# Performance work log

Hardware: AMD Instinct MI355X
Metric: run time of the kernel (lower is better)

## Reference

```python
import jax, jax.numpy as jnp
import numpy as np

D_MODEL = 256; N_HEADS = 8; N_LEVELS = 4; N_POINTS = 4; D_FF = 2048
SHAPES = [(128, 128), (64, 64), (32, 32), (16, 16)]  # (H_l, W_l) per level
LV = sum(h * w for h, w in SHAPES)  # 21760
B = 8; NQ = 900
EPS = 1e-5


def layer_norm(x, s, b):
    m = x.mean(-1, keepdims=True)
    v = x.var(-1, keepdims=True)
    return (x - m) * jax.lax.rsqrt(v + EPS) * s + b


def mha(q, k, v, in_w, in_b, out_w, out_b):
    # torch nn.MultiheadAttention, batch_first, eval mode (no dropout)
    Bq, Lq, C = q.shape
    h = N_HEADS; d = C // h
    wq, wk, wv = jnp.split(in_w, 3, axis=0)
    bq, bk, bv = jnp.split(in_b, 3)
    qh = (q @ wq.T + bq).reshape(Bq, Lq, h, d)
    kh = (k @ wk.T + bk).reshape(Bq, -1, h, d)
    vh = (v @ wv.T + bv).reshape(Bq, -1, h, d)
    scale = jnp.asarray(1.0 / np.sqrt(d), q.dtype)
    attn = jax.nn.softmax(jnp.einsum('bqhd,bkhd->bhqk', qh, kh) * scale, axis=-1)
    o = jnp.einsum('bhqk,bkhd->bqhd', attn, vh).reshape(Bq, Lq, C)
    return o @ out_w.T + out_b


def deform_attn(query, ref, memory, spatial_shapes, val_w, val_b, off_w, off_b, aw_w, aw_b, co_w, co_b):
    # MSDeformAttn forward (eval): offsets/weights from query, bilinear sample value per level/point
    Bq, Lq, C = query.shape
    h, L, P = N_HEADS, N_LEVELS, N_POINTS
    dh = C // h
    value = (memory @ val_w.T + val_b).reshape(Bq, -1, h, dh)  # (B, Lv, h, dh)
    off = (query @ off_w.T + off_b).reshape(Bq, Lq, h, L, P, 2)
    aw = jax.nn.softmax((query @ aw_w.T + aw_b).reshape(Bq, Lq, h, L * P), axis=-1)
    aw = aw.reshape(Bq, Lq, h, L, P)
    # normalizer = (W_l, H_l) per level
    normalizer = spatial_shapes[:, ::-1].astype(query.dtype)
    loc = ref[:, :, None, :, None, :] + off / normalizer[None, None, None, :, None, :]  # (B,Lq,h,L,P,2)
    out = jnp.zeros((Bq, h, Lq, dh), query.dtype)
    start = 0
    for l, (Hl, Wl) in enumerate(SHAPES):
        v_l = value[:, start:start + Hl * Wl].transpose(0, 2, 1, 3)  # (B,h,Hl*Wl,dh)
        start += Hl * Wl
        xy = loc[:, :, :, l]  # (B,Lq,h,P,2) normalized in [0,1]
        # grid_sample align_corners=False pixel coords
        x = xy[..., 0] * Wl - 0.5
        y = xy[..., 1] * Hl - 0.5
        x0 = jnp.floor(x); y0 = jnp.floor(y)
        wx = x - x0; wy = y - y0
        acc = jnp.zeros((Bq, h, Lq * P, dh), query.dtype)
        for dx, dy, w in ((0, 0, (1 - wx) * (1 - wy)), (1, 0, wx * (1 - wy)),
                          (0, 1, (1 - wx) * wy), (1, 1, wx * wy)):
            xi = x0 + dx; yi = y0 + dy
            valid = (xi >= 0) & (xi <= Wl - 1) & (yi >= 0) & (yi <= Hl - 1)
            xi = jnp.clip(xi, 0, Wl - 1).astype(jnp.int32)
            yi = jnp.clip(yi, 0, Hl - 1).astype(jnp.int32)
            idx = (yi * Wl + xi).transpose(0, 2, 1, 3).reshape(Bq, h, Lq * P)
            g = jnp.take_along_axis(v_l, idx[..., None], axis=2)  # (B,h,Lq*P,dh)
            wgt = (w * valid).transpose(0, 2, 1, 3).reshape(Bq, h, Lq * P)
            acc = acc + g * wgt[..., None]
        acc = acc.reshape(Bq, h, Lq, P, dh)
        wl = aw[:, :, :, l].transpose(0, 2, 1, 3)  # (B,h,Lq,P)
        out = out + jnp.einsum('bhqpd,bhqp->bhqd', acc, wl)
    out = out.transpose(0, 2, 1, 3).reshape(Bq, Lq, C)
    return out @ co_w.T + co_b


def forward(tgt, memory, query_pos, reference_points, sa_in_w, sa_in_b, sa_out_w, sa_out_b,
            off_w, off_b, aw_w, aw_b, val_w, val_b, co_w, co_b,
            l1_w, l1_b, l2_w, l2_b, ln1_s, ln1_b, ln2_s, ln2_b, ln3_s, ln3_b, spatial_shapes):
    q = tgt + query_pos  # with_pos_embed; eval mode: no group_detr split, no dropout
    tgt2 = mha(q, q, tgt, sa_in_w, sa_in_b, sa_out_w, sa_out_b)
    tgt = layer_norm(tgt + tgt2, ln1_s, ln1_b)
    tgt2 = deform_attn(tgt + query_pos, reference_points, memory, spatial_shapes,
                       val_w, val_b, off_w, off_b, aw_w, aw_b, co_w, co_b)
    tgt = layer_norm(tgt + tgt2, ln2_s, ln2_b)
    tgt2 = jax.nn.relu(tgt @ l1_w.T + l1_b) @ l2_w.T + l2_b
    return layer_norm(tgt + tgt2, ln3_s, ln3_b)


def setup_inputs():
    key = jax.random.key(0)
    ks = jax.random.split(key, 16)
    C = D_MODEL
    f = lambda i, shape, s=0.02: jax.random.normal(ks[i], shape, jnp.float32) * s
    HLP = N_HEADS * N_LEVELS * N_POINTS
    return {
        'tgt': f(0, (B, NQ, C), 1.0),
        'memory': f(1, (B, LV, C), 1.0),
        'query_pos': f(2, (B, NQ, C), 1.0),
        'reference_points': jax.random.uniform(ks[3], (B, NQ, N_LEVELS, 2), jnp.float32),
        'sa_in_w': f(4, (3 * C, C)), 'sa_in_b': jnp.zeros((3 * C,), jnp.float32),
        'sa_out_w': f(5, (C, C)), 'sa_out_b': jnp.zeros((C,), jnp.float32),
        'off_w': f(6, (HLP * 2, C)), 'off_b': f(7, (HLP * 2,), 0.5),
        'aw_w': f(8, (HLP, C)), 'aw_b': jnp.zeros((HLP,), jnp.float32),
        'val_w': f(9, (C, C)), 'val_b': jnp.zeros((C,), jnp.float32),
        'co_w': f(10, (C, C)), 'co_b': jnp.zeros((C,), jnp.float32),
        'l1_w': f(11, (D_FF, C)), 'l1_b': jnp.zeros((D_FF,), jnp.float32),
        'l2_w': f(12, (C, D_FF)), 'l2_b': jnp.zeros((C,), jnp.float32),
        'ln1_s': jnp.ones((C,), jnp.float32), 'ln1_b': jnp.zeros((C,), jnp.float32),
        'ln2_s': jnp.ones((C,), jnp.float32), 'ln2_b': jnp.zeros((C,), jnp.float32),
        'ln3_s': jnp.ones((C,), jnp.float32), 'ln3_b': jnp.zeros((C,), jnp.float32),
        'spatial_shapes': jnp.asarray(SHAPES, jnp.int32),
        'level_start_index': jnp.asarray(np.cumsum([0] + [h * w for h, w in SHAPES[:-1]]), jnp.int32),
    }


def reference(tgt, memory, query_pos, reference_points, sa_in_w, sa_in_b, sa_out_w, sa_out_b,
              off_w, off_b, aw_w, aw_b, val_w, val_b, co_w, co_b,
              l1_w, l1_b, l2_w, l2_b, ln1_s, ln1_b, ln2_s, ln2_b, ln3_s, ln3_b,
              spatial_shapes, level_start_index):
    return forward(tgt, memory, query_pos, reference_points, sa_in_w, sa_in_b, sa_out_w, sa_out_b,
                   off_w, off_b, aw_w, aw_b, val_w, val_b, co_w, co_b,
                   l1_w, l1_b, l2_w, l2_b, ln1_s, ln1_b, ln2_s, ln2_b, ln3_s, ln3_b, spatial_shapes)
```

## Files before the change

### kernel.cpp

```cpp
#include <hip/hip_runtime.h>
#include <hip/hip_bf16.h>

#define NQL 900
#define CDIM 256
#define BDIM 8
#define LVTOT 21760

typedef __bf16 bf16x8 __attribute__((ext_vector_type(8)));
typedef float f32x4 __attribute__((ext_vector_type(4)));
typedef uint u32x4 __attribute__((ext_vector_type(4)));
typedef uint u32x2 __attribute__((ext_vector_type(2)));

__device__ __forceinline__ ushort f2bf(float x) {
  uint u = __builtin_bit_cast(uint, x);
  u += 0x7fff + ((u >> 16) & 1);
  return (ushort)(u >> 16);
}

template <bool ABF16, bool AADD, bool RELU, bool OUTBF16>
__global__ __launch_bounds__(256, 4) void mgemm_kernel(const void* __restrict__ Ap,
                                                       const float* __restrict__ A2p,
                                                       const float* __restrict__ W,
                                                       const float* __restrict__ bias,
                                                       void* __restrict__ Cout,
                                                       int M, int N, int K) {
  __shared__ ushort smem[10240];
  ushort* As = smem;
  ushort* Bs = smem + 5120;
  const int tid = threadIdx.x;
  const int m0 = blockIdx.y * 128, n0 = blockIdx.x * 128;
  const int wv = tid >> 6;
  const int wm = (wv >> 1) * 64, wn = (wv & 1) * 64;
  const int lane = tid & 63;
  const int lr = lane & 15, kq = lane >> 4;

  f32x4 acc[4][4] = {};
  float4 pa[2][2], pb[2][2];
  u32x4 pa16[2];

  auto load_tiles = [&](int k0) {
#pragma unroll
    for (int it = 0; it < 2; ++it) {
      int idx = it * 256 + tid;
      int r = idx >> 2, s = (idx & 3) << 3;
      int gm = min(m0 + r, M - 1);
      if constexpr (ABF16) {
        pa16[it] = *(const u32x4*)((const ushort*)Ap + (size_t)gm * K + k0 + s);
      } else {
        const float* ap = (const float*)Ap + (size_t)gm * K + k0 + s;
        pa[it][0] = *(const float4*)ap;
        pa[it][1] = *(const float4*)(ap + 4);
        if constexpr (AADD) {
          const float* ap2 = A2p + (size_t)gm * K + k0 + s;
          float4 q0 = *(const float4*)ap2;
          float4 q1 = *(const float4*)(ap2 + 4);
          pa[it][0].x += q0.x; pa[it][0].y += q0.y; pa[it][0].z += q0.z; pa[it][0].w += q0.w;
          pa[it][1].x += q1.x; pa[it][1].y += q1.y; pa[it][1].z += q1.z; pa[it][1].w += q1.w;
        }
      }
      int gn = min(n0 + r, N - 1);
      const float* wp = W + (size_t)gn * K + k0 + s;
      pb[it][0] = *(const float4*)wp;
      pb[it][1] = *(const float4*)(wp + 4);
    }
  };

  auto store_tiles = [&]() {
#pragma unroll
    for (int it = 0; it < 2; ++it) {
      int idx = it * 256 + tid;
      int r = idx >> 2, s = (idx & 3) << 3;
      u32x4 u;
      if constexpr (ABF16) {
        u = pa16[it];
      } else {
        u.x = f2bf(pa[it][0].x) | ((uint)f2bf(pa[it][0].y) << 16);
        u.y = f2bf(pa[it][0].z) | ((uint)f2bf(pa[it][0].w) << 16);
        u.z = f2bf(pa[it][1].x) | ((uint)f2bf(pa[it][1].y) << 16);
        u.w = f2bf(pa[it][1].z) | ((uint)f2bf(pa[it][1].w) << 16);
      }
      *(u32x4*)&As[r * 40 + s] = u;
      u32x4 w;
      w.x = f2bf(pb[it][0].x) | ((uint)f2bf(pb[it][0].y) << 16);
      w.y = f2bf(pb[it][0].z) | ((uint)f2bf(pb[it][0].w) << 16);
      w.z = f2bf(pb[it][1].x) | ((uint)f2bf(pb[it][1].y) << 16);
      w.w = f2bf(pb[it][1].z) | ((uint)f2bf(pb[it][1].w) << 16);
      *(u32x4*)&Bs[r * 40 + s] = w;
    }
  };

  load_tiles(0);
  for (int k0 = 0; k0 < K; k0 += 32) {
    store_tiles();
    __syncthreads();
    if (k0 + 32 < K) load_tiles(k0 + 32);
    bf16x8 af[4], bq[4];
#pragma unroll
    for (int m = 0; m < 4; ++m)
      af[m] = __builtin_bit_cast(bf16x8, *(const u32x4*)&As[(wm + m * 16 + lr) * 40 + kq * 8]);
#pragma unroll
    for (int n = 0; n < 4; ++n)
      bq[n] = __builtin_bit_cast(bf16x8, *(const u32x4*)&Bs[(wn + n * 16 + lr) * 40 + kq * 8]);
#pragma unroll
    for (int m = 0; m < 4; ++m)
#pragma unroll
      for (int n = 0; n < 4; ++n)
        acc[m][n] = __builtin_amdgcn_mfma_f32_16x16x32_bf16(af[m], bq[n], acc[m][n], 0, 0, 0);
    __syncthreads();
  }

  if constexpr (OUTBF16) {
    ushort* Cs = smem;
#pragma unroll
    for (int p = 0; p < 2; ++p) {
      __syncthreads();
      if (wm == p * 64) {
#pragma unroll
        for (int n = 0; n < 4; ++n) {
          int col = wn + n * 16 + lr;
          float bv = bias[n0 + col];
#pragma unroll
          for (int m = 0; m < 4; ++m)
#pragma unroll
            for (int j = 0; j < 4; ++j) {
              float v = acc[m][n][j] + bv;
              if (RELU) v = fmaxf(v, 0.f);
              Cs[(m * 16 + kq * 4 + j) * 136 + col] = f2bf(v);
            }
        }
      }
      __syncthreads();
#pragma unroll
      for (int it = 0; it < 4; ++it) {
        int idx = it * 256 + tid;
        int r = idx >> 4, c = (idx & 15) * 8;
        int grow = m0 + p * 64 + r;
        if (grow < M) {
          u32x4 u = *(const u32x4*)&Cs[r * 136 + c];
          *(u32x4*)((ushort*)Cout + (size_t)grow * N + n0 + c) = u;
        }
      }
    }
  } else {
#pragma unroll
    for (int n = 0; n < 4; ++n) {
      int gcol = n0 + wn + n * 16 + lr;
      float bv = bias[gcol];
#pragma unroll
      for (int m = 0; m < 4; ++m) {
        int rbase = m0 + wm + m * 16 + kq * 4;
#pragma unroll
        for (int j = 0; j < 4; ++j) {
          int grow = rbase + j;
          if (grow >= M) continue;
          float v = acc[m][n][j] + bv;
          if (RELU) v = fmaxf(v, 0.f);
          ((float*)Cout)[(size_t)grow * N + gcol] = v;
        }
      }
    }
  }
}

template <bool ABF16, bool AADD, bool RELU, bool HASRES, bool OUTBF16>
__global__ __launch_bounds__(256, 4) void mgemm64_kernel(const void* __restrict__ Ap,
                                                         const float* __restrict__ A2p,
                                                         const float* __restrict__ W,
                                                         const float* __restrict__ bias,
                                                         const float* __restrict__ Rres,
                                                         void* __restrict__ Cout,
                                                         int M, int N, int K) {
  __shared__ ushort smem[5120];
  ushort* As = smem;
  ushort* Bs = smem + 2560;
  const int tid = threadIdx.x;
  const int m0 = blockIdx.y * 64, n0 = blockIdx.x * 64;
  const int wv = tid >> 6, lane = tid & 63;
  const int wm = (wv >> 1) * 32, wn = (wv & 1) * 32;
  const int lr = lane & 15, kq = lane >> 4;

  f32x4 acc[2][2] = {};
  float4 pa[2], pb[2];
  u32x4 pa16;

  auto load_tiles = [&](int k0) {
    int r = tid >> 2, s = (tid & 3) << 3;
    int gm = min(m0 + r, M - 1);
    if constexpr (ABF16) {
      pa16 = *(const u32x4*)((const ushort*)Ap + (size_t)gm * K + k0 + s);
    } else {
      const float* ap = (const float*)Ap + (size_t)gm * K + k0 + s;
      pa[0] = *(const float4*)ap;
      pa[1] = *(const float4*)(ap + 4);
      if constexpr (AADD) {
        const float* ap2 = A2p + (size_t)gm * K + k0 + s;
        float4 q0 = *(const float4*)ap2;
        float4 q1 = *(const float4*)(ap2 + 4);
        pa[0].x += q0.x; pa[0].y += q0.y; pa[0].z += q0.z; pa[0].w += q0.w;
        pa[1].x += q1.x; pa[1].y += q1.y; pa[1].z += q1.z; pa[1].w += q1.w;
      }
    }
    int gn = min(n0 + r, N - 1);
    const float* wp = W + (size_t)gn * K + k0 + s;
    pb[0] = *(const float4*)wp;
    pb[1] = *(const float4*)(wp + 4);
  };

  auto store_tiles = [&]() {
    int r = tid >> 2, s = (tid & 3) << 3;
    u32x4 u;
    if constexpr (ABF16) {
      u = pa16;
    } else {
      u.x = f2bf(pa[0].x) | ((uint)f2bf(pa[0].y) << 16);
      u.y = f2bf(pa[0].z) | ((uint)f2bf(pa[0].w) << 16);
      u.z = f2bf(pa[1].x) | ((uint)f2bf(pa[1].y) << 16);
      u.w = f2bf(pa[1].z) | ((uint)f2bf(pa[1].w) << 16);
    }
    *(u32x4*)&As[r * 40 + s] = u;
    u32x4 w;
    w.x = f2bf(pb[0].x) | ((uint)f2bf(pb[0].y) << 16);
    w.y = f2bf(pb[0].z) | ((uint)f2bf(pb[0].w) << 16);
    w.z = f2bf(pb[1].x) | ((uint)f2bf(pb[1].y) << 16);
    w.w = f2bf(pb[1].z) | ((uint)f2bf(pb[1].w) << 16);
    *(u32x4*)&Bs[r * 40 + s] = w;
  };

  load_tiles(0);
  for (int k0 = 0; k0 < K; k0 += 32) {
    store_tiles();
    __syncthreads();
    if (k0 + 32 < K) load_tiles(k0 + 32);
    bf16x8 af[2], bq[2];
#pragma unroll
    for (int m = 0; m < 2; ++m)
      af[m] = __builtin_bit_cast(bf16x8, *(const u32x4*)&As[(wm + m * 16 + lr) * 40 + kq * 8]);
#pragma unroll
    for (int n = 0; n < 2; ++n)
      bq[n] = __builtin_bit_cast(bf16x8, *(const u32x4*)&Bs[(wn + n * 16 + lr) * 40 + kq * 8]);
#pragma unroll
    for (int m = 0; m < 2; ++m)
#pragma unroll
      for (int n = 0; n < 2; ++n)
        acc[m][n] = __builtin_amdgcn_mfma_f32_16x16x32_bf16(af[m], bq[n], acc[m][n], 0, 0, 0);
    __syncthreads();
  }

  if constexpr (OUTBF16) {
    ushort* Cs = smem;
    __syncthreads();
#pragma unroll
    for (int n = 0; n < 2; ++n) {
      int col = wn + n * 16 + lr;
      float bv = bias[n0 + col];
#pragma unroll
      for (int m = 0; m < 2; ++m)
#pragma unroll
        for (int j = 0; j < 4; ++j) {
          float v = acc[m][n][j] + bv;
          if (RELU) v = fmaxf(v, 0.f);
          Cs[(wm + m * 16 + kq * 4 + j) * 72 + col] = f2bf(v);
        }
    }
    __syncthreads();
#pragma unroll
    for (int it = 0; it < 2; ++it) {
      int idx = it * 256 + tid;
      int r = idx >> 3, c = (idx & 7) * 8;
      int grow = m0 + r;
      if (grow < M) {
        u32x4 u = *(const u32x4*)&Cs[r * 72 + c];
        *(u32x4*)((ushort*)Cout + (size_t)grow * N + n0 + c) = u;
      }
    }
  } else {
#pragma unroll
    for (int n = 0; n < 2; ++n) {
      int gcol = n0 + wn + n * 16 + lr;
      float bv = bias[gcol];
#pragma unroll
      for (int m = 0; m < 2; ++m) {
        int rbase = m0 + wm + m * 16 + kq * 4;
#pragma unroll
        for (int j = 0; j < 4; ++j) {
          int grow = rbase + j;
          if (grow >= M) continue;
          float v = acc[m][n][j] + bv;
          if (HASRES) v += Rres[(size_t)grow * N + gcol];
          if (RELU) v = fmaxf(v, 0.f);
          ((float*)Cout)[(size_t)grow * N + gcol] = v;
        }
      }
    }
  }
}

template <bool ABF16, bool OUTBF16>
__global__ __launch_bounds__(256, 2) void mgemm256_kernel(const void* __restrict__ Ap,
                                                          const float* __restrict__ W,
                                                          const float* __restrict__ bias,
                                                          void* __restrict__ Cout,
                                                          int M, int K) {
  __shared__ ushort smem[16896];
  ushort* As = smem;
  ushort* Bs = smem + 2560;
  const int tid = threadIdx.x;
  const int m0 = blockIdx.x * 64;
  const int wv = tid >> 6;
  const int lane = tid & 63;
  const int lr = lane & 15, kq = lane >> 4;

  f32x4 acc[16] = {};
  float4 pa[2];
  u32x4 pa16;
  float4 pb[4][2];

  auto load_tiles = [&](int k0) {
    {
      int r = tid >> 2, s = (tid & 3) << 3;
      int gm = min(m0 + r, M - 1);
      if constexpr (ABF16) {
        pa16 = *(const u32x4*)((const ushort*)Ap + (size_t)gm * K + k0 + s);
      } else {
        const float* ap = (const float*)Ap + (size_t)gm * K + k0 + s;
        pa[0] = *(const float4*)ap;
        pa[1] = *(const float4*)(ap + 4);
      }
    }
#pragma unroll
    for (int it = 0; it < 4; ++it) {
      int idx = it * 256 + tid;
      int r = idx >> 2, s = (idx & 3) << 3;
      const float* wp = W + (size_t)r * K + k0 + s;
      pb[it][0] = *(const float4*)wp;
      pb[it][1] = *(const float4*)(wp + 4);
    }
  };

  auto store_tiles = [&]() {
    {
      int r = tid >> 2, s = (tid & 3) << 3;
      u32x4 u;
      if constexpr (ABF16) {
        u = pa16;
      } else {
        u.x = f2bf(pa[0].x) | ((uint)f2bf(pa[0].y) << 16);
        u.y = f2bf(pa[0].z) | ((uint)f2bf(pa[0].w) << 16);
        u.z = f2bf(pa[1].x) | ((uint)f2bf(pa[1].y) << 16);
        u.w = f2bf(pa[1].z) | ((uint)f2bf(pa[1].w) << 16);
      }
      *(u32x4*)&As[r * 40 + s] = u;
    }
#pragma unroll
    for (int it = 0; it < 4; ++it) {
      int idx = it * 256 + tid;
      int r = idx >> 2, s = (idx & 3) << 3;
      u32x4 w;
      w.x = f2bf(pb[it][0].x) | ((uint)f2bf(pb[it][0].y) << 16);
      w.y = f2bf(pb[it][0].z) | ((uint)f2bf(pb[it][0].w) << 16);
      w.z = f2bf(pb[it][1].x) | ((uint)f2bf(pb[it][1].y) << 16);
      w.w = f2bf(pb[it][1].z) | ((uint)f2bf(pb[it][1].w) << 16);
      *(u32x4*)&Bs[r * 40 + s] = w;
    }
  };

  load_tiles(0);
  for (int k0 = 0; k0 < K; k0 += 32) {
    store_tiles();
    __syncthreads();
    if (k0 + 32 < K) load_tiles(k0 + 32);
    bf16x8 af = __builtin_bit_cast(bf16x8, *(const u32x4*)&As[(wv * 16 + lr) * 40 + kq * 8]);
#pragma unroll
    for (int ng = 0; ng < 16; ++ng) {
      bf16x8 bq = __builtin_bit_cast(bf16x8, *(const u32x4*)&Bs[(ng * 16 + lr) * 40 + kq * 8]);
      acc[ng] = __builtin_amdgcn_mfma_f32_16x16x32_bf16(af, bq, acc[ng], 0, 0, 0);
    }
    __syncthreads();
  }

  if constexpr (OUTBF16) {
    ushort* Cs = smem;
#pragma unroll
    for (int nf = 0; nf < 16; ++nf) {
      int col = nf * 16 + lr;
      float bv = bias[col];
#pragma unroll
      for (int j = 0; j < 4; ++j) {
        int row = wv * 16 + kq * 4 + j;
        Cs[row * 264 + col] = f2bf(acc[nf][j] + bv);
      }
    }
    __syncthreads();
#pragma unroll
    for (int it = 0; it < 8; ++it) {
      int idx = it * 256 + tid;
      int r = idx >> 5, c = (idx & 31) * 8;
      int grow = m0 + r;
      if (grow < M) {
        u32x4 u = *(const u32x4*)&Cs[r * 264 + c];
        *(u32x4*)((ushort*)Cout + (size_t)grow * 256 + c) = u;
      }
    }
  } else {
#pragma unroll
    for (int nf = 0; nf < 16; ++nf) {
      int col = nf * 16 + lr;
      float bv = bias[col];
#pragma unroll
      for (int j = 0; j < 4; ++j) {
        int grow = m0 + wv * 16 + kq * 4 + j;
        if (grow < M)
          ((float*)Cout)[(size_t)grow * 256 + col] = acc[nf][j] + bv;
      }
    }
  }
}

__global__ __launch_bounds__(256) void vt_kernel(const ushort* __restrict__ tmp_v,
                                                 ushort* __restrict__ vt) {
  __shared__ ushort Ls[64 * 40];
  const int qt = blockIdx.x;
  const int bh = blockIdx.y;
  const int b = bh >> 3, h = bh & 7;
  const int tid = threadIdx.x;
  const int q0 = qt * 64;
  {
    int r = tid >> 2, c = (tid & 3) * 8;
    int gq = min(q0 + r, NQL - 1);
    u32x4 u = *(const u32x4*)(tmp_v + ((size_t)(b * NQL + gq) * 256) + h * 32 + c);
    *(u32x4*)&Ls[r * 40 + c] = u;
  }
  __syncthreads();
  {
    int d = tid >> 3, qw = (tid & 7) * 8;
    u32x4 u;
    uint w[8];
#pragma unroll
    for (int j = 0; j < 8; ++j) w[j] = Ls[(qw + j) * 40 + d];
    u.x = w[0] | (w[1] << 16);
    u.y = w[2] | (w[3] << 16);
    u.z = w[4] | (w[5] << 16);
    u.w = w[6] | (w[7] << 16);
    *(u32x4*)(vt + ((size_t)(bh * 32 + d) * 960) + q0 + qw) = u;
  }
}

__global__ __launch_bounds__(256, 2) void fattn_kernel(const ushort* __restrict__ qk,
                                                       const ushort* __restrict__ vt,
                                                       float* __restrict__ out) {
  __shared__ ushort Ks[64 * 40];
  __shared__ ushort Vs[32 * 72];
  __shared__ ushort Ps[4][16 * 72];
  const int qt = blockIdx.x, bh = blockIdx.y;
  const int b = bh >> 3, h = bh & 7;
  const int tid = threadIdx.x;
  const int wv = tid >> 6, lane = tid & 63;
  const int lq = lane & 15, hi = lane >> 4;
  const int q0 = qt * 64 + wv * 16;
  const float SC = 0.17677669529663689f;

  bf16x8 qfrag;
  {
    int qrow = min(q0 + lq, NQL - 1);
    qfrag = __builtin_bit_cast(bf16x8,
        *(const u32x4*)(qk + (size_t)(b * NQL + qrow) * 512 + h * 32 + hi * 8));
  }

  f32x4 o0 = {}, o1 = {};
  float mrow = -1e30f, lrow = 0.f;

  for (int kt = 0; kt < 15; ++kt) {
    const int k0 = kt * 64;
    __syncthreads();
    {
      int r = tid >> 2, c = (tid & 3) * 8;
      int gk = min(k0 + r, NQL - 1);
      u32x4 u = *(const u32x4*)(qk + (size_t)(b * NQL + gk) * 512 + 256 + h * 32 + c);
      *(u32x4*)&Ks[r * 40 + c] = u;
    }
    {
      int r = tid >> 3, c = (tid & 7) * 8;
      u32x4 u = *(const u32x4*)(vt + (size_t)(bh * 32 + r) * 960 + k0 + c);
      *(u32x4*)&Vs[r * 72 + c] = u;
    }
    __syncthreads();

    f32x4 st[4];
#pragma unroll
    for (int mt = 0; mt < 4; ++mt) {
      bf16x8 kf = __builtin_bit_cast(bf16x8, *(const u32x4*)&Ks[(mt * 16 + lq) * 40 + hi * 8]);
      f32x4 z = {};
      st[mt] = __builtin_amdgcn_mfma_f32_16x16x32_bf16(kf, qfrag, z, 0, 0, 0);
    }
    float sv[4][4];
    float lmax = -1e30f;
#pragma unroll
    for (int mt = 0; mt < 4; ++mt)
#pragma unroll
      for (int j = 0; j < 4; ++j) {
        int key = k0 + mt * 16 + hi * 4 + j;
        float v = st[mt][j] * SC;
        v = (key < NQL) ? v : -1e30f;
        sv[mt][j] = v;
        lmax = fmaxf(lmax, v);
      }
    lmax = fmaxf(lmax, __shfl_xor(lmax, 16));
    lmax = fmaxf(lmax, __shfl_xor(lmax, 32));
    float mnew = fmaxf(mrow, lmax);
    float rs = __expf(mrow - mnew);
    float lsum = 0.f;
    uint pw[4][2];
#pragma unroll
    for (int mt = 0; mt < 4; ++mt) {
      float p0 = __expf(sv[mt][0] - mnew);
      float p1 = __expf(sv[mt][1] - mnew);
      float p2 = __expf(sv[mt][2] - mnew);
      float p3 = __expf(sv[mt][3] - mnew);
      lsum += (p0 + p1) + (p2 + p3);
      pw[mt][0] = f2bf(p0) | ((uint)f2bf(p1) << 16);
      pw[mt][1] = f2bf(p2) | ((uint)f2bf(p3) << 16);
    }
    lsum += __shfl_xor(lsum, 16);
    lsum += __shfl_xor(lsum, 32);
    lrow = lrow * rs + lsum;
    mrow = mnew;
#pragma unroll
    for (int j = 0; j < 4; ++j) {
      float rsj = __shfl(rs, hi * 4 + j);
      o0[j] *= rsj;
      o1[j] *= rsj;
    }
#pragma unroll
    for (int mt = 0; mt < 4; ++mt) {
      u32x2 u;
      u.x = pw[mt][0];
      u.y = pw[mt][1];
      *(u32x2*)&Ps[wv][lq * 72 + mt * 16 + hi * 4] = u;
    }
#pragma unroll
    for (int k2 = 0; k2 < 2; ++k2) {
      bf16x8 pa = __builtin_bit_cast(bf16x8, *(const u32x4*)&Ps[wv][lq * 72 + k2 * 32 + hi * 8]);
      bf16x8 vb0 = __builtin_bit_cast(bf16x8, *(const u32x4*)&Vs[(0 * 16 + lq) * 72 + k2 * 32 + hi * 8]);
      bf16x8 vb1 = __builtin_bit_cast(bf16x8, *(const u32x4*)&Vs[(1 * 16 + lq) * 72 + k2 * 32 + hi * 8]);
      o0 = __builtin_amdgcn_mfma_f32_16x16x32_bf16(pa, vb0, o0, 0, 0, 0);
      o1 = __builtin_amdgcn_mfma_f32_16x16x32_bf16(pa, vb1, o1, 0, 0, 0);
    }
  }

#pragma unroll
  for (int j = 0; j < 4; ++j) {
    float lj = __shfl(lrow, hi * 4 + j);
    float inv = 1.f / lj;
    int gq = q0 + hi * 4 + j;
    if (gq < NQL) {
      float* op = out + (size_t)(b * NQL + gq) * 256 + h * 32;
      op[lq] = o0[j] * inv;
      op[16 + lq] = o1[j] * inv;
    }
  }
}

__global__ __launch_bounds__(256) void ln_kernel(const float* __restrict__ x,
                                                 const float* __restrict__ s,
                                                 const float* __restrict__ bb,
                                                 float* __restrict__ out) {
  int row = blockIdx.x, tid = threadIdx.x;
  float v = x[(size_t)row * 256 + tid];
  __shared__ float r1[256], r2[256];
  r1[tid] = v;
  r2[tid] = v * v;
  __syncthreads();
  for (int st = 128; st > 0; st >>= 1) {
    if (tid < st) { r1[tid] += r1[tid + st]; r2[tid] += r2[tid + st]; }
    __syncthreads();
  }
  float m = r1[0] * (1.f / 256);
  float var = r2[0] * (1.f / 256) - m * m;
  out[(size_t)row * 256 + tid] = (v - m) * rsqrtf(var + 1e-5f) * s[tid] + bb[tid];
}

__global__ __launch_bounds__(128) void awsm_kernel(float* __restrict__ aw) {
  int row = blockIdx.x, tid = threadIdx.x;
  float v = aw[(size_t)row * 128 + tid];
  float m = v;
  for (int d = 1; d < 16; d <<= 1) m = fmaxf(m, __shfl_xor(m, d));
  float e = expf(v - m);
  float ssum = e;
  for (int d = 1; d < 16; d <<= 1) ssum += __shfl_xor(ssum, d);
  aw[(size_t)row * 128 + tid] = e / ssum;
}

__global__ __launch_bounds__(256) void deform_kernel(const __hip_bfloat16* __restrict__ value,
                                                     const float* __restrict__ offb,
                                                     const float* __restrict__ awb,
                                                     const float* __restrict__ refp,
                                                     float* __restrict__ dfout) {
  const int Hs[4] = {128, 64, 32, 16};
  const int Stl[4] = {0, 16384, 20480, 21504};
  int row = blockIdx.x;
  int b = row / NQL;
  int tid = threadIdx.x;
  int h = tid >> 5, d = tid & 31;
  const float* off = offb + (size_t)row * 256;
  const float* aw = awb + (size_t)row * 128;
  const float* ref = refp + (size_t)row * 8;
  const __hip_bfloat16* vb = value + (size_t)b * LVTOT * 256 + h * 32 + d;
  float acc = 0.f;
#pragma unroll
  for (int l = 0; l < 4; ++l) {
    int Wi = Hs[l], Hi = Hs[l];
    float Wl = (float)Wi, Hl = (float)Hi;
    int st = Stl[l];
    float rx = ref[l * 2 + 0], ry = ref[l * 2 + 1];
#pragma unroll
    for (int p = 0; p < 4; ++p) {
      int oi = ((h * 4 + l) * 4 + p) * 2;
      float x = (rx + off[oi] / Wl) * Wl - 0.5f;
      float y = (ry + off[oi + 1] / Hl) * Hl - 0.5f;
      float w = aw[h * 16 + l * 4 + p];
      float x0f = floorf(x), y0f = floorf(y);
      float wx = x - x0f, wy = y - y0f;
      int xi0 = (int)x0f, yi0 = (int)y0f;
      float samp = 0.f;
#pragma unroll
      for (int dy = 0; dy < 2; ++dy) {
#pragma unroll
        for (int dx = 0; dx < 2; ++dx) {
          int xi = xi0 + dx, yi = yi0 + dy;
          float tw = (dx ? wx : 1.f - wx) * (dy ? wy : 1.f - wy);
          bool valid = (xi >= 0) && (xi < Wi) && (yi >= 0) && (yi < Hi);
          int xc = min(max(xi, 0), Wi - 1);
          int yc = min(max(yi, 0), Hi - 1);
          float vv = __bfloat162float(vb[(size_t)(st + yc * Wi + xc) * 256]);
          samp += valid ? tw * vv : 0.f;
        }
      }
      acc = fmaf(w, samp, acc);
    }
  }
  dfout[(size_t)row * 256 + tid] = acc;
}

extern "C" void kernel_launch(void* const* d_in, const int* in_sizes, int n_in,
                              void* d_out, int out_size, void* d_ws, size_t ws_size,
                              hipStream_t stream) {
  const float* tgt = (const float*)d_in[0];
  const float* memory = (const float*)d_in[1];
  const float* qpos = (const float*)d_in[2];
  const float* refp = (const float*)d_in[3];
  const float* sa_in_w = (const float*)d_in[4];
  const float* sa_in_b = (const float*)d_in[5];
  const float* sa_out_w = (const float*)d_in[6];
  const float* sa_out_b = (const float*)d_in[7];
  const float* off_w = (const float*)d_in[8];
  const float* off_b = (const float*)d_in[9];
  const float* aw_w = (const float*)d_in[10];
  const float* aw_b = (const float*)d_in[11];
  const float* val_w = (const float*)d_in[12];
  const float* val_b = (const float*)d_in[13];
  const float* co_w = (const float*)d_in[14];
  const float* co_b = (const float*)d_in[15];
  const float* l1_w = (const float*)d_in[16];
  const float* l1_b = (const float*)d_in[17];
  const float* l2_w = (const float*)d_in[18];
  const float* l2_b = (const float*)d_in[19];
  const float* ln1_s = (const float*)d_in[20];
  const float* ln1_b = (const float*)d_in[21];
  const float* ln2_s = (const float*)d_in[22];
  const float* ln2_b = (const float*)d_in[23];
  const float* ln3_s = (const float*)d_in[24];
  const float* ln3_b = (const float*)d_in[25];

  float* ws = (float*)d_ws;
  const size_t E = (size_t)BDIM * NQL * CDIM;
  ushort* vt = (ushort*)(ws + E);
  float* attn_o = ws + 4 * E;
  ushort* tmp_qk = (ushort*)(ws + 5 * E);
  ushort* tmp_v = (ushort*)(ws + 7 * E);
  float* sa_out = ws + 5 * E;
  float* offb = ws + E;
  float* awb = ws + 2 * E;
  float* dfout = ws + 3 * E;
  float* co_out = ws + 4 * E;
  ushort* hidden = (ushort*)ws;
  float* ffn_o = ws + 4 * E;
  float* tgt1 = ws + 8 * E;
  float* tgt2 = ws + 9 * E;
  ushort* valbf = (ushort*)(ws + 11 * E);

  const int M = BDIM * NQL;
  const int MT = (M + 127) / 128;
  const int M64 = (M + 63) / 64;
  dim3 blk(256);

  mgemm64_kernel<false, true, false, false, true><<<dim3(8, M64), blk, 0, stream>>>(
      tgt, qpos, sa_in_w, sa_in_b, nullptr, tmp_qk, M, 512, 256);
  mgemm64_kernel<false, false, false, false, true><<<dim3(4, M64), blk, 0, stream>>>(
      tgt, nullptr, sa_in_w + 512 * 256, sa_in_b + 512, nullptr, tmp_v, M, 256, 256);
  vt_kernel<<<dim3(15, 64), blk, 0, stream>>>(tmp_v, vt);
  fattn_kernel<<<dim3(15, 64), blk, 0, stream>>>(tmp_qk, vt, attn_o);
  mgemm64_kernel<false, false, false, true, false><<<dim3(4, M64), blk, 0, stream>>>(
      attn_o, nullptr, sa_out_w, sa_out_b, tgt, sa_out, M, 256, 256);
  ln_kernel<<<M, blk, 0, stream>>>(sa_out, ln1_s, ln1_b, tgt1);
  mgemm256_kernel<false, true><<<(BDIM * LVTOT) / 64, blk, 0, stream>>>(
      memory, val_w, val_b, valbf, BDIM * LVTOT, 256);
  mgemm64_kernel<false, true, false, false, false><<<dim3(4, M64), blk, 0, stream>>>(
      tgt1, qpos, off_w, off_b, nullptr, offb, M, 256, 256);
  mgemm64_kernel<false, true, false, false, false><<<dim3(2, M64), blk, 0, stream>>>(
      tgt1, qpos, aw_w, aw_b, nullptr, awb, M, 128, 256);
  awsm_kernel<<<M, 128, 0, stream>>>(awb);
  deform_kernel<<<M, blk, 0, stream>>>((const __hip_bfloat16*)valbf, offb, awb, refp, dfout);
  mgemm64_kernel<false, false, false, true, false><<<dim3(4, M64), blk, 0, stream>>>(
      dfout, nullptr, co_w, co_b, tgt1, co_out, M, 256, 256);
  ln_kernel<<<M, blk, 0, stream>>>(co_out, ln2_s, ln2_b, tgt2);
  mgemm_kernel<false, false, true, true><<<dim3(16, MT), blk, 0, stream>>>(
      tgt2, nullptr, l1_w, l1_b, hidden, M, 2048, 256);
  mgemm64_kernel<true, false, false, true, false><<<dim3(4, M64), blk, 0, stream>>>(
      hidden, nullptr, l2_w, l2_b, tgt2, ffn_o, M, 256, 2048);
  ln_kernel<<<M, blk, 0, stream>>>(ffn_o, ln3_s, ln3_b, (float*)d_out);
}
```

Baseline: 353.7 us.

## Fuse attention-weight softmax into GEMM epilogue, shrink value-GEMM LDS, warp-per-row layernorm

Three changes. The attention-weight softmax is folded into the aw projection GEMM epilogue using 16-lane shuffle reductions, which removes the separate awsm kernel launch and one round trip through global memory. The value-projection GEMM stages its bf16 output through LDS in two 32-row halves, cutting shared memory so launch bounds can allow 4 blocks per CU instead of 2. LayerNorm now uses one wavefront per row with float4 loads and shuffle reductions in place of a block-wide LDS tree reduction. The fused softmax relies on each 16-column group lining up with one head's 16 weights, and the staged epilogue adds an extra barrier.

```diff
diff --git a/kernel.cpp b/kernel.cpp
--- a/kernel.cpp
+++ b/kernel.cpp
@@ -162,7 +162,7 @@
   }
 }
 
-template <bool ABF16, bool AADD, bool RELU, bool HASRES, bool OUTBF16>
+template <bool ABF16, bool AADD, bool RELU, bool HASRES, bool DOSM, bool OUTBF16>
 __global__ __launch_bounds__(256, 4) void mgemm64_kernel(const void* __restrict__ Ap,
                                                          const float* __restrict__ A2p,
                                                          const float* __restrict__ W,
@@ -284,8 +284,18 @@
 #pragma unroll
         for (int j = 0; j < 4; ++j) {
           int grow = rbase + j;
+          float v = acc[m][n][j] + bv;
+          if constexpr (DOSM) {
+            float gmax = v;
+#pragma unroll
+            for (int w = 1; w < 16; w <<= 1) gmax = fmaxf(gmax, __shfl_xor(gmax, w));
+            float e = __expf(v - gmax);
+            float gs = e;
+#pragma unroll
+            for (int w = 1; w < 16; w <<= 1) gs += __shfl_xor(gs, w);
+            v = e / gs;
+          }
           if (grow >= M) continue;
-          float v = acc[m][n][j] + bv;
           if (HASRES) v += Rres[(size_t)grow * N + gcol];
           if (RELU) v = fmaxf(v, 0.f);
           ((float*)Cout)[(size_t)grow * N + gcol] = v;
@@ -296,12 +306,12 @@
 }
 
 template <bool ABF16, bool OUTBF16>
-__global__ __launch_bounds__(256, 2) void mgemm256_kernel(const void* __restrict__ Ap,
+__global__ __launch_bounds__(256, 4) void mgemm256_kernel(const void* __restrict__ Ap,
                                                           const float* __restrict__ W,
                                                           const float* __restrict__ bias,
                                                           void* __restrict__ Cout,
                                                           int M, int K) {
-  __shared__ ushort smem[16896];
+  __shared__ ushort smem[12800];
   ushort* As = smem;
   ushort* Bs = smem + 2560;
   const int tid = threadIdx.x;
@@ -381,24 +391,30 @@
   if constexpr (OUTBF16) {
     ushort* Cs = smem;
 #pragma unroll
-    for (int nf = 0; nf < 16; ++nf) {
-      int col = nf * 16 + lr;
-      float bv = bias[col];
-#pragma unroll
-      for (int j = 0; j < 4; ++j) {
-        int row = wv * 16 + kq * 4 + j;
-        Cs[row * 264 + col] = f2bf(acc[nf][j] + bv);
-      }
-    }
-    __syncthreads();
-#pragma unroll
-    for (int it = 0; it < 8; ++it) {
-      int idx = it * 256 + tid;
-      int r = idx >> 5, c = (idx & 31) * 8;
-      int grow = m0 + r;
-      if (grow < M) {
-        u32x4 u = *(const u32x4*)&Cs[r * 264 + c];
-        *(u32x4*)((ushort*)Cout + (size_t)grow * 256 + c) = u;
+    for (int p = 0; p < 2; ++p) {
+      __syncthreads();
+      if ((wv >> 1) == p) {
+#pragma unroll
+        for (int nf = 0; nf < 16; ++nf) {
+          int col = nf * 16 + lr;
+          float bv = bias[col];
+#pragma unroll
+          for (int j = 0; j < 4; ++j) {
+            int row = (wv & 1) * 16 + kq * 4 + j;
+            Cs[row * 264 + col] = f2bf(acc[nf][j] + bv);
+          }
+        }
+      }
+      __syncthreads();
+#pragma unroll
+      for (int it = 0; it < 4; ++it) {
+        int idx = it * 256 + tid;
+        int r = idx >> 5, c = (idx & 31) * 8;
+        int grow = m0 + p * 32 + r;
+        if (grow < M) {
+          u32x4 u = *(const u32x4*)&Cs[r * 264 + c];
+          *(u32x4*)((ushort*)Cout + (size_t)grow * 256 + c) = u;
+        }
       }
     }
   } else {
@@ -563,31 +579,29 @@
 __global__ __launch_bounds__(256) void ln_kernel(const float* __restrict__ x,
                                                  const float* __restrict__ s,
                                                  const float* __restrict__ bb,
-                                                 float* __restrict__ out) {
-  int row = blockIdx.x, tid = threadIdx.x;
-  float v = x[(size_t)row * 256 + tid];
-  __shared__ float r1[256], r2[256];
-  r1[tid] = v;
-  r2[tid] = v * v;
-  __syncthreads();
-  for (int st = 128; st > 0; st >>= 1) {
-    if (tid < st) { r1[tid] += r1[tid + st]; r2[tid] += r2[tid + st]; }
-    __syncthreads();
-  }
-  float m = r1[0] * (1.f / 256);
-  float var = r2[0] * (1.f / 256) - m * m;
-  out[(size_t)row * 256 + tid] = (v - m) * rsqrtf(var + 1e-5f) * s[tid] + bb[tid];
-}
-
-__global__ __launch_bounds__(128) void awsm_kernel(float* __restrict__ aw) {
-  int row = blockIdx.x, tid = threadIdx.x;
-  float v = aw[(size_t)row * 128 + tid];
-  float m = v;
-  for (int d = 1; d < 16; d <<= 1) m = fmaxf(m, __shfl_xor(m, d));
-  float e = expf(v - m);
-  float ssum = e;
-  for (int d = 1; d < 16; d <<= 1) ssum += __shfl_xor(ssum, d);
-  aw[(size_t)row * 128 + tid] = e / ssum;
+                                                 float* __restrict__ out, int M) {
+  const int wv = threadIdx.x >> 6, lane = threadIdx.x & 63;
+  const int row = blockIdx.x * 4 + wv;
+  if (row >= M) return;
+  const float4 v = *(const float4*)(x + (size_t)row * 256 + lane * 4);
+  float s1 = (v.x + v.y) + (v.z + v.w);
+  float s2 = (v.x * v.x + v.y * v.y) + (v.z * v.z + v.w * v.w);
+#pragma unroll
+  for (int w = 1; w < 64; w <<= 1) {
+    s1 += __shfl_xor(s1, w);
+    s2 += __shfl_xor(s2, w);
+  }
+  float mean = s1 * (1.f / 256.f);
+  float var = s2 * (1.f / 256.f) - mean * mean;
+  float inv = rsqrtf(var + 1e-5f);
+  float4 sc = *(const float4*)(s + lane * 4);
+  float4 bv = *(const float4*)(bb + lane * 4);
+  float4 o;
+  o.x = (v.x - mean) * inv * sc.x + bv.x;
+  o.y = (v.y - mean) * inv * sc.y + bv.y;
+  o.z = (v.z - mean) * inv * sc.z + bv.z;
+  o.w = (v.w - mean) * inv * sc.w + bv.w;
+  *(float4*)(out + (size_t)row * 256 + lane * 4) = o;
 }
 
 __global__ __launch_bounds__(256) void deform_kernel(const __hip_bfloat16* __restrict__ value,
@@ -691,31 +705,31 @@
   const int M = BDIM * NQL;
   const int MT = (M + 127) / 128;
   const int M64 = (M + 63) / 64;
+  const int LNG = (M + 3) / 4;
   dim3 blk(256);
 
-  mgemm64_kernel<false, true, false, false, true><<<dim3(8, M64), blk, 0, stream>>>(
+  mgemm64_kernel<false, true, false, false, false, true><<<dim3(8, M64), blk, 0, stream>>>(
       tgt, qpos, sa_in_w, sa_in_b, nullptr, tmp_qk, M, 512, 256);
-  mgemm64_kernel<false, false, false, false, true><<<dim3(4, M64), blk, 0, stream>>>(
+  mgemm64_kernel<false, false, false, false, false, true><<<dim3(4, M64), blk, 0, stream>>>(
       tgt, nullptr, sa_in_w + 512 * 256, sa_in_b + 512, nullptr, tmp_v, M, 256, 256);
   vt_kernel<<<dim3(15, 64), blk, 0, stream>>>(tmp_v, vt);
   fattn_kernel<<<dim3(15, 64), blk, 0, stream>>>(tmp_qk, vt, attn_o);
-  mgemm64_kernel<false, false, false, true, false><<<dim3(4, M64), blk, 0, stream>>>(
+  mgemm64_kernel<false, false, false, true, false, false><<<dim3(4, M64), blk, 0, stream>>>(
       attn_o, nullptr, sa_out_w, sa_out_b, tgt, sa_out, M, 256, 256);
-  ln_kernel<<<M, blk, 0, stream>>>(sa_out, ln1_s, ln1_b, tgt1);
+  ln_kernel<<<LNG, blk, 0, stream>>>(sa_out, ln1_s, ln1_b, tgt1, M);
   mgemm256_kernel<false, true><<<(BDIM * LVTOT) / 64, blk, 0, stream>>>(
       memory, val_w, val_b, valbf, BDIM * LVTOT, 256);
-  mgemm64_kernel<false, true, false, false, false><<<dim3(4, M64), blk, 0, stream>>>(
+  mgemm64_kernel<false, true, false, false, false, false><<<dim3(4, M64), blk, 0, stream>>>(
       tgt1, qpos, off_w, off_b, nullptr, offb, M, 256, 256);
-  mgemm64_kernel<false, true, false, false, false><<<dim3(2, M64), blk, 0, stream>>>(
+  mgemm64_kernel<false, true, false, false, true, false><<<dim3(2, M64), blk, 0, stream>>>(
       tgt1, qpos, aw_w, aw_b, nullptr, awb, M, 128, 256);
-  awsm_kernel<<<M, 128, 0, stream>>>(awb);
   deform_kernel<<<M, blk, 0, stream>>>((const __hip_bfloat16*)valbf, offb, awb, refp, dfout);
-  mgemm64_kernel<false, false, false, true, false><<<dim3(4, M64), blk, 0, stream>>>(
+  mgemm64_kernel<false, false, false, true, false, false><<<dim3(4, M64), blk, 0, stream>>>(
       dfout, nullptr, co_w, co_b, tgt1, co_out, M, 256, 256);
-  ln_kernel<<<M, blk, 0, stream>>>(co_out, ln2_s, ln2_b, tgt2);
+  ln_kernel<<<LNG, blk, 0, stream>>>(co_out, ln2_s, ln2_b, tgt2, M);
   mgemm_kernel<false, false, true, true><<<dim3(16, MT), blk, 0, stream>>>(
       tgt2, nullptr, l1_w, l1_b, hidden, M, 2048, 256);
-  mgemm64_kernel<true, false, false, true, false><<<dim3(4, M64), blk, 0, stream>>>(
+  mgemm64_kernel<true, false, false, true, false, false><<<dim3(4, M64), blk, 0, stream>>>(
       hidden, nullptr, l2_w, l2_b, tgt2, ffn_o, M, 256, 2048);
-  ln_kernel<<<M, blk, 0, stream>>>(ffn_o, ln3_s, ln3_b, (float*)d_out);
-}
+  ln_kernel<<<LNG, blk, 0, stream>>>(ffn_o, ln3_s, ln3_b, (float*)d_out, M);
+}
```

Measured after the change: 359.4 us. Within noise of the previous version (+1.6%).
